# Performance work log

Measured on AMD Instinct MI355X. Metric: run time of the kernel, lower is better.

Reference implementation:

```python
import jax, jax.numpy as jnp
import numpy as np

N = 50000          # nodes
E = 400000         # edges (avg degree 8)
F_IN = 128
F_OUT = 128
H = 4
C = F_OUT // H     # 32
SCALE = np.sqrt(C).astype(np.float32)
EPS = 1e-5


def _linear_params(key, fan_out, fan_in):
    # torch nn.Linear default init: U(-1/sqrt(fan_in), 1/sqrt(fan_in))
    bound = 1.0 / np.sqrt(fan_in)
    kw, kb = jax.random.split(key)
    W = jax.random.uniform(kw, (fan_out, fan_in), minval=-bound, maxval=bound, dtype=jnp.float32)
    b = jax.random.uniform(kb, (fan_out,), minval=-bound, maxval=bound, dtype=jnp.float32)
    return W, b


def setup_inputs() -> dict:
    key = jax.random.key(0)
    ks = jax.random.split(key, 12)
    Wq, bq = _linear_params(ks[0], F_OUT, F_IN)
    Wk, bk = _linear_params(ks[1], F_OUT, F_IN)
    Wv, bv = _linear_params(ks[2], F_OUT, F_IN)
    We, be = _linear_params(ks[3], F_OUT, F_IN)
    Wev, bev = _linear_params(ks[4], F_OUT, F_IN)
    Wout, bout = _linear_params(ks[5], F_OUT, F_OUT)
    node_feats = jax.random.normal(ks[6], (N, F_IN), dtype=jnp.float32)
    edge_feats = jax.random.normal(ks[7], (E, F_IN), dtype=jnp.float32)
    src = jax.random.randint(ks[8], (E,), 0, N, dtype=jnp.int32)
    dst = jax.random.randint(ks[9], (E,), 0, N, dtype=jnp.int32)
    return {
        'node_feats': node_feats, 'edge_feats': edge_feats,
        'src': src, 'dst': dst,
        'Wq': Wq, 'bq': bq, 'Wk': Wk, 'bk': bk, 'Wv': Wv, 'bv': bv,
        'We': We, 'be': be, 'Wev': Wev, 'bev': bev, 'Wout': Wout, 'bout': bout,
        'ln_ng': jnp.ones((F_OUT,), jnp.float32), 'ln_nb': jnp.zeros((F_OUT,), jnp.float32),
        'ln_eg': jnp.ones((F_OUT,), jnp.float32), 'ln_eb': jnp.zeros((F_OUT,), jnp.float32),
    }


def _layernorm(x, g, b):
    mu = jnp.mean(x, axis=-1, keepdims=True)
    var = jnp.var(x, axis=-1, keepdims=True)
    return (x - mu) * jax.lax.rsqrt(var + EPS) * g + b


def reference(node_feats, edge_feats, src, dst,
              Wq, bq, Wk, bk, Wv, bv, We, be, Wev, bev, Wout, bout,
              ln_ng, ln_nb, ln_eg, ln_eb):
    # per-node projections, viewed as [N, H, C]
    q = (node_feats @ Wq.T + bq).reshape(N, H, C)
    k = (node_feats @ Wk.T + bk).reshape(N, H, C)
    v = (node_feats @ Wv.T + bv).reshape(N, H, C)
    e = (edge_feats @ We.T + be).reshape(E, H, C)

    # u_dot_v('q','k','score'): per-edge per-head dot -> [E, H, 1]
    score = jnp.einsum('ehc,ehc->eh', q[src], k[dst])[:, :, None]
    m = score / SCALE + e                       # broadcast -> [E, H, C]
    # NOTE: faithful to original — softmax over the HEADS axis (dim=1)
    attn = jax.nn.softmax(m, axis=1)            # [E, H, C]

    # u_mul_e + sum aggregation at destination
    msg = v[src] * attn                         # [E, H, C]
    agg = jax.ops.segment_sum(msg, dst, num_segments=N)   # [N, H, C]

    x = agg.reshape(N, H * C)
    y = m.reshape(E, H * C)
    x = jax.nn.silu(_layernorm(x, ln_ng, ln_nb))
    y = jax.nn.silu(_layernorm(y, ln_eg, ln_eb))
    # residual
    x = (node_feats @ Wout.T + bout) + x
    y = (edge_feats @ Wev.T + bev) + y
    return (x, y)
```

## Files before the change

### kernel.cpp

```cpp
#include <hip/hip_runtime.h>
#include <math.h>

#define NN 50000
#define NE 400000
#define FDIM 128

constexpr float INV_SCALE = 0.17677669529663687f;
constexpr float LN_EPS = 1e-5f;

typedef short bf16x8 __attribute__((ext_vector_type(8)));
typedef float f32x4 __attribute__((ext_vector_type(4)));

static __device__ __forceinline__ short f2bf(float f) {
    unsigned u = __builtin_bit_cast(unsigned, f);
    u += 0x7FFFu + ((u >> 16) & 1u);
    return (short)(u >> 16);
}
static __device__ __forceinline__ float bf2f(short h) {
    unsigned u = ((unsigned)(unsigned short)h) << 16;
    return __builtin_bit_cast(float, u);
}

static __device__ __forceinline__ void load_afrags(const short* At, int w, int l, bf16x8* a) {
    int lr = l & 15, lq = l >> 4;
    int arow = w * 16 + lr;
#pragma unroll
    for (int ks = 0; ks < 4; ++ks) {
        int ch = ks * 4 + lq;
        a[ks] = *(const bf16x8*)(At + arow * FDIM + ((ch ^ (arow & 7)) * 8));
    }
}

static __device__ __forceinline__ void mfma_gemm(const bf16x8* a,
                                                 const short* __restrict__ W,
                                                 const float* __restrict__ bias,
                                                 int lr, int lq, f32x4* acc) {
#pragma unroll
    for (int n = 0; n < 8; ++n) {
        float bb = bias[n * 16 + lr];
        f32x4 t; t[0] = bb; t[1] = bb; t[2] = bb; t[3] = bb;
        acc[n] = t;
#pragma unroll
        for (int ks = 0; ks < 4; ++ks) {
            bf16x8 b = *(const bf16x8*)(W + (n * 16 + lr) * FDIM + ks * 32 + lq * 8);
            acc[n] = __builtin_amdgcn_mfma_f32_16x16x32_bf16(a[ks], b, acc[n], 0, 0, 0);
        }
    }
}

__global__ __launch_bounds__(256) void convert_weights(
    const float* __restrict__ w0, const float* __restrict__ w1,
    const float* __restrict__ w2, const float* __restrict__ w3,
    const float* __restrict__ w4, const float* __restrict__ w5,
    short* __restrict__ out) {
    int idx = blockIdx.x * 256 + threadIdx.x;
    const float* srcs[6] = {w0, w1, w2, w3, w4, w5};
    out[idx] = f2bf(srcs[idx >> 14][idx & 16383]);
}

__global__ __launch_bounds__(256) void hist_kernel(const int* __restrict__ dst,
                                                   int* __restrict__ hist) {
    int e = blockIdx.x * 256 + threadIdx.x;
    if (e < NE) atomicAdd(&hist[dst[e]], 1);
}

__global__ __launch_bounds__(256) void scan_kernel(const int* __restrict__ hist,
                                                   int* __restrict__ cursor) {
    __shared__ int wsum[4];
    __shared__ int srun;
    int tid = threadIdx.x;
    int lane = tid & 63, w = tid >> 6;
    if (tid == 0) srun = 0;
    __syncthreads();
    for (int base = 0; base < NN; base += 256) {
        int i = base + tid;
        int v = (i < NN) ? hist[i] : 0;
        int inc = v;
#pragma unroll
        for (int off = 1; off < 64; off <<= 1) {
            int t = __shfl_up(inc, off);
            if (lane >= off) inc += t;
        }
        if (lane == 63) wsum[w] = inc;
        __syncthreads();
        int wo = 0;
        for (int j = 0; j < w; ++j) wo += wsum[j];
        int run = srun;
        if (i < NN) cursor[i] = run + wo + inc - v;
        __syncthreads();
        if (tid == 255) srun = run + wo + inc;
        __syncthreads();
    }
}

__global__ __launch_bounds__(256) void scatter_kernel(const int* __restrict__ dst,
                                                      int* __restrict__ cursor,
                                                      int* __restrict__ sidx) {
    int e = blockIdx.x * 256 + threadIdx.x;
    if (e < NE) sidx[atomicAdd(&cursor[dst[e]], 1)] = e;
}

__global__ __launch_bounds__(256) void node_proj_kernel(
    const float* __restrict__ nf,
    const short* __restrict__ wq16, const short* __restrict__ wk16,
    const short* __restrict__ wv16, const short* __restrict__ wo16,
    const float* __restrict__ bq, const float* __restrict__ bk,
    const float* __restrict__ bv, const float* __restrict__ bo,
    short* __restrict__ q, short* __restrict__ k, short* __restrict__ v,
    float* __restrict__ xout) {
    __shared__ __align__(16) short At[64 * FDIM];
    int m0  = blockIdx.x * 64;
    int tid = threadIdx.x;
#pragma unroll
    for (int j = 0; j < 4; ++j) {
        int row = (tid >> 4) + j * 16;
        int g   = tid & 15;
        int m   = m0 + row;
        float4 a0 = make_float4(0.f, 0.f, 0.f, 0.f);
        float4 a1 = make_float4(0.f, 0.f, 0.f, 0.f);
        if (m < NN) {
            const float4* p = (const float4*)(nf + (size_t)m * FDIM + g * 8);
            a0 = p[0]; a1 = p[1];
        }
        bf16x8 h;
        h[0] = f2bf(a0.x); h[1] = f2bf(a0.y); h[2] = f2bf(a0.z); h[3] = f2bf(a0.w);
        h[4] = f2bf(a1.x); h[5] = f2bf(a1.y); h[6] = f2bf(a1.z); h[7] = f2bf(a1.w);
        *(bf16x8*)(At + row * FDIM + ((g ^ (row & 7)) * 8)) = h;
    }
    __syncthreads();
    int w = tid >> 6, l = tid & 63;
    int lr = l & 15, lq = l >> 4;
    bf16x8 a[4];
    load_afrags(At, w, l, a);
    f32x4 acc[8];
    const short* Ws[3] = {wq16, wk16, wv16};
    const float* Bs[3] = {bq, bk, bv};
    short*       Os[3] = {q, k, v};
#pragma unroll
    for (int t = 0; t < 3; ++t) {
        mfma_gemm(a, Ws[t], Bs[t], lr, lq, acc);
#pragma unroll
        for (int n = 0; n < 8; ++n)
#pragma unroll
            for (int r = 0; r < 4; ++r) {
                int m = m0 + w * 16 + lq * 4 + r;
                if (m < NN) Os[t][(size_t)m * FDIM + n * 16 + lr] = f2bf(acc[n][r]);
            }
    }
    mfma_gemm(a, wo16, bo, lr, lq, acc);
#pragma unroll
    for (int n = 0; n < 8; ++n)
#pragma unroll
        for (int r = 0; r < 4; ++r) {
            int m = m0 + w * 16 + lq * 4 + r;
            if (m < NN) xout[(size_t)m * FDIM + n * 16 + lr] = acc[n][r];
        }
}

__global__ __launch_bounds__(256) void edge_kernel(
    const float* __restrict__ ef, const int* __restrict__ src, const int* __restrict__ dst,
    const int* __restrict__ sidx,
    const short* __restrict__ we16, const short* __restrict__ wev16,
    const float* __restrict__ be, const float* __restrict__ bev,
    const short* __restrict__ qbf, const short* __restrict__ kbf, const short* __restrict__ vbf,
    const float* __restrict__ ln_eg, const float* __restrict__ ln_eb,
    float* __restrict__ agg, float* __restrict__ yout) {
    __shared__ __align__(16) short At[64 * FDIM];
    __shared__ __align__(16) float sc[64 * 4];
    __shared__ int oL[64], sL[64], dL[64];
    int e0  = blockIdx.x * 64;
    int tid = threadIdx.x;

#pragma unroll
    for (int j = 0; j < 4; ++j) {
        int row = (tid >> 4) + j * 16;
        int g   = tid & 15;
        int o   = sidx[e0 + row];
        const float4* p = (const float4*)(ef + (size_t)o * FDIM + g * 8);
        float4 a0 = p[0], a1 = p[1];
        bf16x8 h;
        h[0] = f2bf(a0.x); h[1] = f2bf(a0.y); h[2] = f2bf(a0.z); h[3] = f2bf(a0.w);
        h[4] = f2bf(a1.x); h[5] = f2bf(a1.y); h[6] = f2bf(a1.z); h[7] = f2bf(a1.w);
        *(bf16x8*)(At + row * FDIM + ((g ^ (row & 7)) * 8)) = h;
    }

    int w = tid >> 6, l = tid & 63;
    {
        int eidx = w * 16 + (l >> 2);
        int h    = l & 3;
        int o    = sidx[e0 + eidx];
        int se = src[o], de = dst[o];
        if (h == 0) { oL[eidx] = o; sL[eidx] = se; dL[eidx] = de; }
        const bf16x8* qp = (const bf16x8*)(qbf + (size_t)se * FDIM + h * 32);
        const bf16x8* kp = (const bf16x8*)(kbf + (size_t)de * FDIM + h * 32);
        float s = 0.f;
#pragma unroll
        for (int i = 0; i < 4; ++i) {
            bf16x8 qa = qp[i], ka = kp[i];
#pragma unroll
            for (int jj = 0; jj < 8; ++jj) s += bf2f(qa[jj]) * bf2f(ka[jj]);
        }
        sc[eidx * 4 + h] = s * INV_SCALE;
    }
    __syncthreads();

    int lr = l & 15, lq = l >> 4;
    bf16x8 a[4];
    load_afrags(At, w, l, a);
    __syncthreads();

    f32x4 me[8], mvv[8];
    mfma_gemm(a, we16, be, lr, lq, me);
    mfma_gemm(a, wev16, bev, lr, lq, mvv);

    int rowb = w * 16 + lq * 4;
    float sr[4][4];
#pragma unroll
    for (int r = 0; r < 4; ++r) {
        f32x4 t = *(const f32x4*)(sc + (rowb + r) * 4);
        sr[r][0] = t[0]; sr[r][1] = t[1]; sr[r][2] = t[2]; sr[r][3] = t[3];
    }
#pragma unroll
    for (int n = 0; n < 8; ++n)
#pragma unroll
        for (int r = 0; r < 4; ++r)
            me[n][r] += sr[r][n >> 1];

    short* attnL = At;
#pragma unroll
    for (int r = 0; r < 4; ++r) {
#pragma unroll
        for (int half = 0; half < 2; ++half) {
            float v0 = me[half][r],     v1 = me[half + 2][r];
            float v2 = me[half + 4][r], v3 = me[half + 6][r];
            float mx = fmaxf(fmaxf(v0, v1), fmaxf(v2, v3));
            float x0 = __expf(v0 - mx), x1 = __expf(v1 - mx);
            float x2 = __expf(v2 - mx), x3 = __expf(v3 - mx);
            float inv = 1.f / (x0 + x1 + x2 + x3);
            float at[4] = {x0 * inv, x1 * inv, x2 * inv, x3 * inv};
#pragma unroll
            for (int h = 0; h < 4; ++h)
                attnL[(rowb + r) * FDIM + (2 * h + half) * 16 + lr] = f2bf(at[h]);
        }
    }

#pragma unroll
    for (int r = 0; r < 4; ++r) {
        float sum1 = 0.f, sum2 = 0.f;
#pragma unroll
        for (int n = 0; n < 8; ++n) { float t = me[n][r]; sum1 += t; sum2 += t * t; }
#pragma unroll
        for (int off = 1; off < 16; off <<= 1) {
            sum1 += __shfl_xor(sum1, off);
            sum2 += __shfl_xor(sum2, off);
        }
        float mean = sum1 * (1.f / 128.f);
        float var  = sum2 * (1.f / 128.f) - mean * mean;
        float rstd = rsqrtf(var + LN_EPS);
        int orow = oL[rowb + r];
#pragma unroll
        for (int n = 0; n < 8; ++n) {
            int col = n * 16 + lr;
            float t  = (me[n][r] - mean) * rstd * ln_eg[col] + ln_eb[col];
            float si = t / (1.f + __expf(-t));
            yout[(size_t)orow * FDIM + col] = si + mvv[n][r];
        }
    }
    __syncthreads();

    {
        int c  = tid & 127;
        int hh = tid >> 7;
        int j0 = hh * 32, j1 = j0 + 32;
        float acc = 0.f;
        int cur = dL[j0];
        for (int j = j0; j < j1; ++j) {
            int d = dL[j];
            if (d != cur) {
                unsafeAtomicAdd(&agg[(size_t)cur * FDIM + c], acc);
                acc = 0.f; cur = d;
            }
            float vv = bf2f(vbf[(size_t)sL[j] * FDIM + c]);
            float aa = bf2f(attnL[j * FDIM + c]);
            acc += vv * aa;
        }
        unsafeAtomicAdd(&agg[(size_t)cur * FDIM + c], acc);
    }
}

__global__ __launch_bounds__(256) void node_epilogue(
    const float* __restrict__ agg,
    const float* __restrict__ ln_ng, const float* __restrict__ ln_nb,
    float* __restrict__ xout) {
    int row = blockIdx.x * 4 + (threadIdx.x >> 6);
    if (row >= NN) return;
    int l = threadIdx.x & 63;
    float2 aa = *(const float2*)(agg + (size_t)row * FDIM + l * 2);
    float sum1 = aa.x + aa.y, sum2 = aa.x * aa.x + aa.y * aa.y;
#pragma unroll
    for (int off = 1; off < 64; off <<= 1) {
        sum1 += __shfl_xor(sum1, off);
        sum2 += __shfl_xor(sum2, off);
    }
    float mean = sum1 * (1.f / 128.f);
    float var  = sum2 * (1.f / 128.f) - mean * mean;
    float rstd = rsqrtf(var + LN_EPS);
    float2 gg = *(const float2*)(ln_ng + l * 2);
    float2 bb = *(const float2*)(ln_nb + l * 2);
    float t0 = (aa.x - mean) * rstd * gg.x + bb.x;
    float t1 = (aa.y - mean) * rstd * gg.y + bb.y;
    float s0 = t0 / (1.f + __expf(-t0));
    float s1 = t1 / (1.f + __expf(-t1));
    float2 o = *(const float2*)(xout + (size_t)row * FDIM + l * 2);
    o.x += s0;
    o.y += s1;
    *(float2*)(xout + (size_t)row * FDIM + l * 2) = o;
}

extern "C" void kernel_launch(void* const* d_in, const int* in_sizes, int n_in,
                              void* d_out, int out_size, void* d_ws, size_t ws_size,
                              hipStream_t stream) {
    const float* nf   = (const float*)d_in[0];
    const float* ef   = (const float*)d_in[1];
    const int*   src  = (const int*)d_in[2];
    const int*   dst  = (const int*)d_in[3];
    const float* Wq   = (const float*)d_in[4];  const float* bq   = (const float*)d_in[5];
    const float* Wk   = (const float*)d_in[6];  const float* bk   = (const float*)d_in[7];
    const float* Wv   = (const float*)d_in[8];  const float* bv   = (const float*)d_in[9];
    const float* We   = (const float*)d_in[10]; const float* be   = (const float*)d_in[11];
    const float* Wev  = (const float*)d_in[12]; const float* bev  = (const float*)d_in[13];
    const float* Wout = (const float*)d_in[14]; const float* bout = (const float*)d_in[15];
    const float* ln_ng = (const float*)d_in[16]; const float* ln_nb = (const float*)d_in[17];
    const float* ln_eg = (const float*)d_in[18]; const float* ln_eb = (const float*)d_in[19];

    float* xout = (float*)d_out;
    float* yout = xout + (size_t)NN * FDIM;

    char* ws = (char*)d_ws;
    short* qbf  = (short*)ws;                                   ws += (size_t)NN * FDIM * 2;
    short* kbf  = (short*)ws;                                   ws += (size_t)NN * FDIM * 2;
    short* vbf  = (short*)ws;                                   ws += (size_t)NN * FDIM * 2;
    float* agg  = (float*)ws;                                   ws += (size_t)NN * FDIM * 4;
    short* w16  = (short*)ws;                                   ws += (size_t)6 * 16384 * 2;
    int*   hist = (int*)ws;                                     ws += (size_t)NN * 4;
    int*   curs = (int*)ws;                                     ws += (size_t)NN * 4;
    int*   sidx = (int*)ws;                                     ws += (size_t)NE * 4;
    short* wq16  = w16;
    short* wk16  = w16 + 16384;
    short* wv16  = w16 + 32768;
    short* we16  = w16 + 49152;
    short* wev16 = w16 + 65536;
    short* wo16  = w16 + 81920;

    hipMemsetAsync(agg, 0, (size_t)NN * FDIM * sizeof(float), stream);
    hipMemsetAsync(hist, 0, (size_t)NN * sizeof(int), stream);
    convert_weights<<<384, 256, 0, stream>>>(Wq, Wk, Wv, We, Wev, Wout, w16);
    hist_kernel<<<(NE + 255) / 256, 256, 0, stream>>>(dst, hist);
    scan_kernel<<<1, 256, 0, stream>>>(hist, curs);
    scatter_kernel<<<(NE + 255) / 256, 256, 0, stream>>>(dst, curs, sidx);
    node_proj_kernel<<<(NN + 63) / 64, 256, 0, stream>>>(
        nf, wq16, wk16, wv16, wo16, bq, bk, bv, bout, qbf, kbf, vbf, xout);
    edge_kernel<<<NE / 64, 256, 0, stream>>>(
        ef, src, dst, sidx, we16, wev16, be, bev, qbf, kbf, vbf, ln_eg, ln_eb, agg, yout);
    node_epilogue<<<(NN + 3) / 4, 256, 0, stream>>>(agg, ln_ng, ln_nb, xout);
}
```

Measured before the change: 969.3 us.

## Replace atomic scatter aggregation with CSR pull-based node aggregation and parallel scan

The edge kernel now processes edges in original order, with coalesced edge-feature reads and output writes, and stores bf16 attention weights to a workspace buffer. A new node kernel pulls messages per destination node through the CSR index and fuses the sum with the layernorm epilogue. This removes the float atomics, the agg memset and the permuted edge writes. The single-block serial scan is replaced by a three-kernel parallel scan. In exchange it writes and re-reads roughly 100MB of attention data and adds dependent gather loads per edge in the node kernel.

```diff
diff --git a/kernel.cpp b/kernel.cpp
--- a/kernel.cpp
+++ b/kernel.cpp
@@ -4,6 +4,7 @@
 #define NN 50000
 #define NE 400000
 #define FDIM 128
+#define NB 196
 
 constexpr float INV_SCALE = 0.17677669529663687f;
 constexpr float LN_EPS = 1e-5f;
@@ -64,32 +65,52 @@
     if (e < NE) atomicAdd(&hist[dst[e]], 1);
 }
 
-__global__ __launch_bounds__(256) void scan_kernel(const int* __restrict__ hist,
-                                                   int* __restrict__ cursor) {
+__global__ __launch_bounds__(256) void scanA_kernel(const int* __restrict__ hist,
+                                                    int* __restrict__ row_start,
+                                                    int* __restrict__ bsum) {
     __shared__ int wsum[4];
-    __shared__ int srun;
-    int tid = threadIdx.x;
-    int lane = tid & 63, w = tid >> 6;
-    if (tid == 0) srun = 0;
-    __syncthreads();
-    for (int base = 0; base < NN; base += 256) {
-        int i = base + tid;
-        int v = (i < NN) ? hist[i] : 0;
-        int inc = v;
-#pragma unroll
-        for (int off = 1; off < 64; off <<= 1) {
-            int t = __shfl_up(inc, off);
-            if (lane >= off) inc += t;
-        }
-        if (lane == 63) wsum[w] = inc;
-        __syncthreads();
-        int wo = 0;
-        for (int j = 0; j < w; ++j) wo += wsum[j];
-        int run = srun;
-        if (i < NN) cursor[i] = run + wo + inc - v;
-        __syncthreads();
-        if (tid == 255) srun = run + wo + inc;
-        __syncthreads();
+    int tid = threadIdx.x, lane = tid & 63, w = tid >> 6;
+    int i = blockIdx.x * 256 + tid;
+    int v = (i < NN) ? hist[i] : 0;
+    int inc = v;
+#pragma unroll
+    for (int off = 1; off < 64; off <<= 1) {
+        int t = __shfl_up(inc, off);
+        if (lane >= off) inc += t;
+    }
+    if (lane == 63) wsum[w] = inc;
+    __syncthreads();
+    int wo = 0;
+    for (int j = 0; j < w; ++j) wo += wsum[j];
+    if (i < NN) row_start[i] = wo + inc - v;
+    if (tid == 255) bsum[blockIdx.x] = wo + inc;
+}
+
+__global__ __launch_bounds__(256) void scanB_kernel(int* __restrict__ bsum) {
+    __shared__ int wsum[4];
+    int tid = threadIdx.x, lane = tid & 63, w = tid >> 6;
+    int v = (tid < NB) ? bsum[tid] : 0;
+    int inc = v;
+#pragma unroll
+    for (int off = 1; off < 64; off <<= 1) {
+        int t = __shfl_up(inc, off);
+        if (lane >= off) inc += t;
+    }
+    if (lane == 63) wsum[w] = inc;
+    __syncthreads();
+    int wo = 0;
+    for (int j = 0; j < w; ++j) wo += wsum[j];
+    if (tid < NB) bsum[tid] = wo + inc - v;
+}
+
+__global__ __launch_bounds__(256) void scanC_kernel(int* __restrict__ row_start,
+                                                    const int* __restrict__ bsum,
+                                                    int* __restrict__ cursor) {
+    int i = blockIdx.x * 256 + threadIdx.x;
+    if (i < NN) {
+        int s = row_start[i] + bsum[blockIdx.x];
+        row_start[i] = s;
+        cursor[i] = s;
     }
 }
 
@@ -157,17 +178,15 @@
         }
 }
 
-__global__ __launch_bounds__(256) void edge_kernel(
+__global__ __launch_bounds__(256) void edge_m_kernel(
     const float* __restrict__ ef, const int* __restrict__ src, const int* __restrict__ dst,
-    const int* __restrict__ sidx,
     const short* __restrict__ we16, const short* __restrict__ wev16,
     const float* __restrict__ be, const float* __restrict__ bev,
-    const short* __restrict__ qbf, const short* __restrict__ kbf, const short* __restrict__ vbf,
+    const short* __restrict__ qbf, const short* __restrict__ kbf,
     const float* __restrict__ ln_eg, const float* __restrict__ ln_eb,
-    float* __restrict__ agg, float* __restrict__ yout) {
+    short* __restrict__ attn, float* __restrict__ yout) {
     __shared__ __align__(16) short At[64 * FDIM];
     __shared__ __align__(16) float sc[64 * 4];
-    __shared__ int oL[64], sL[64], dL[64];
     int e0  = blockIdx.x * 64;
     int tid = threadIdx.x;
 
@@ -175,8 +194,7 @@
     for (int j = 0; j < 4; ++j) {
         int row = (tid >> 4) + j * 16;
         int g   = tid & 15;
-        int o   = sidx[e0 + row];
-        const float4* p = (const float4*)(ef + (size_t)o * FDIM + g * 8);
+        const float4* p = (const float4*)(ef + (size_t)(e0 + row) * FDIM + g * 8);
         float4 a0 = p[0], a1 = p[1];
         bf16x8 h;
         h[0] = f2bf(a0.x); h[1] = f2bf(a0.y); h[2] = f2bf(a0.z); h[3] = f2bf(a0.w);
@@ -188,9 +206,8 @@
     {
         int eidx = w * 16 + (l >> 2);
         int h    = l & 3;
-        int o    = sidx[e0 + eidx];
-        int se = src[o], de = dst[o];
-        if (h == 0) { oL[eidx] = o; sL[eidx] = se; dL[eidx] = de; }
+        int eg   = e0 + eidx;
+        int se = src[eg], de = dst[eg];
         const bf16x8* qp = (const bf16x8*)(qbf + (size_t)se * FDIM + h * 32);
         const bf16x8* kp = (const bf16x8*)(kbf + (size_t)de * FDIM + h * 32);
         float s = 0.f;
@@ -214,17 +231,13 @@
     mfma_gemm(a, wev16, bev, lr, lq, mvv);
 
     int rowb = w * 16 + lq * 4;
-    float sr[4][4];
 #pragma unroll
     for (int r = 0; r < 4; ++r) {
         f32x4 t = *(const f32x4*)(sc + (rowb + r) * 4);
-        sr[r][0] = t[0]; sr[r][1] = t[1]; sr[r][2] = t[2]; sr[r][3] = t[3];
-    }
-#pragma unroll
-    for (int n = 0; n < 8; ++n)
-#pragma unroll
-        for (int r = 0; r < 4; ++r)
-            me[n][r] += sr[r][n >> 1];
+#pragma unroll
+        for (int n = 0; n < 8; ++n)
+            me[n][r] += ((const float*)&t)[n >> 1];
+    }
 
     short* attnL = At;
 #pragma unroll
@@ -257,46 +270,52 @@
         float mean = sum1 * (1.f / 128.f);
         float var  = sum2 * (1.f / 128.f) - mean * mean;
         float rstd = rsqrtf(var + LN_EPS);
-        int orow = oL[rowb + r];
+        int eg = e0 + rowb + r;
 #pragma unroll
         for (int n = 0; n < 8; ++n) {
             int col = n * 16 + lr;
             float t  = (me[n][r] - mean) * rstd * ln_eg[col] + ln_eb[col];
             float si = t / (1.f + __expf(-t));
-            yout[(size_t)orow * FDIM + col] = si + mvv[n][r];
-        }
-    }
-    __syncthreads();
-
-    {
-        int c  = tid & 127;
-        int hh = tid >> 7;
-        int j0 = hh * 32, j1 = j0 + 32;
-        float acc = 0.f;
-        int cur = dL[j0];
-        for (int j = j0; j < j1; ++j) {
-            int d = dL[j];
-            if (d != cur) {
-                unsafeAtomicAdd(&agg[(size_t)cur * FDIM + c], acc);
-                acc = 0.f; cur = d;
-            }
-            float vv = bf2f(vbf[(size_t)sL[j] * FDIM + c]);
-            float aa = bf2f(attnL[j * FDIM + c]);
-            acc += vv * aa;
-        }
-        unsafeAtomicAdd(&agg[(size_t)cur * FDIM + c], acc);
-    }
-}
-
-__global__ __launch_bounds__(256) void node_epilogue(
-    const float* __restrict__ agg,
+            yout[(size_t)eg * FDIM + col] = si + mvv[n][r];
+        }
+    }
+    __syncthreads();
+
+#pragma unroll
+    for (int j = 0; j < 4; ++j) {
+        int row = (tid >> 4) + j * 16;
+        int g   = tid & 15;
+        *(bf16x8*)(attn + (size_t)(e0 + row) * FDIM + g * 8) =
+            *(const bf16x8*)(attnL + row * FDIM + g * 8);
+    }
+}
+
+__global__ __launch_bounds__(256) void node_agg_kernel(
+    const int* __restrict__ row_start, const int* __restrict__ hist,
+    const int* __restrict__ sidx, const int* __restrict__ src,
+    const short* __restrict__ attn, const short* __restrict__ vbf,
     const float* __restrict__ ln_ng, const float* __restrict__ ln_nb,
     float* __restrict__ xout) {
-    int row = blockIdx.x * 4 + (threadIdx.x >> 6);
-    if (row >= NN) return;
-    int l = threadIdx.x & 63;
-    float2 aa = *(const float2*)(agg + (size_t)row * FDIM + l * 2);
-    float sum1 = aa.x + aa.y, sum2 = aa.x * aa.x + aa.y * aa.y;
+    int tid = threadIdx.x;
+    int w = tid >> 6, l = tid & 63;
+    int n = blockIdx.x * 4 + w;
+    if (n >= NN) return;
+    int start = row_start[n];
+    int deg   = hist[n];
+    float a0 = 0.f, a1 = 0.f;
+    for (int j = 0; j < deg; ++j) {
+        int e = sidx[start + j];
+        int s = src[e];
+        unsigned av = *(const unsigned*)(attn + (size_t)e * FDIM + l * 2);
+        unsigned vv = *(const unsigned*)(vbf  + (size_t)s * FDIM + l * 2);
+        float alo = __builtin_bit_cast(float, av << 16);
+        float ahi = __builtin_bit_cast(float, av & 0xFFFF0000u);
+        float vlo = __builtin_bit_cast(float, vv << 16);
+        float vhi = __builtin_bit_cast(float, vv & 0xFFFF0000u);
+        a0 += alo * vlo;
+        a1 += ahi * vhi;
+    }
+    float sum1 = a0 + a1, sum2 = a0 * a0 + a1 * a1;
 #pragma unroll
     for (int off = 1; off < 64; off <<= 1) {
         sum1 += __shfl_xor(sum1, off);
@@ -307,14 +326,14 @@
     float rstd = rsqrtf(var + LN_EPS);
     float2 gg = *(const float2*)(ln_ng + l * 2);
     float2 bb = *(const float2*)(ln_nb + l * 2);
-    float t0 = (aa.x - mean) * rstd * gg.x + bb.x;
-    float t1 = (aa.y - mean) * rstd * gg.y + bb.y;
+    float t0 = (a0 - mean) * rstd * gg.x + bb.x;
+    float t1 = (a1 - mean) * rstd * gg.y + bb.y;
     float s0 = t0 / (1.f + __expf(-t0));
     float s1 = t1 / (1.f + __expf(-t1));
-    float2 o = *(const float2*)(xout + (size_t)row * FDIM + l * 2);
+    float2 o = *(const float2*)(xout + (size_t)n * FDIM + l * 2);
     o.x += s0;
     o.y += s1;
-    *(float2*)(xout + (size_t)row * FDIM + l * 2) = o;
+    *(float2*)(xout + (size_t)n * FDIM + l * 2) = o;
 }
 
 extern "C" void kernel_launch(void* const* d_in, const int* in_sizes, int n_in,
@@ -337,14 +356,16 @@
     float* yout = xout + (size_t)NN * FDIM;
 
     char* ws = (char*)d_ws;
-    short* qbf  = (short*)ws;                                   ws += (size_t)NN * FDIM * 2;
-    short* kbf  = (short*)ws;                                   ws += (size_t)NN * FDIM * 2;
-    short* vbf  = (short*)ws;                                   ws += (size_t)NN * FDIM * 2;
-    float* agg  = (float*)ws;                                   ws += (size_t)NN * FDIM * 4;
-    short* w16  = (short*)ws;                                   ws += (size_t)6 * 16384 * 2;
-    int*   hist = (int*)ws;                                     ws += (size_t)NN * 4;
-    int*   curs = (int*)ws;                                     ws += (size_t)NN * 4;
-    int*   sidx = (int*)ws;                                     ws += (size_t)NE * 4;
+    short* qbf  = (short*)ws;   ws += (size_t)NN * FDIM * 2;
+    short* kbf  = (short*)ws;   ws += (size_t)NN * FDIM * 2;
+    short* vbf  = (short*)ws;   ws += (size_t)NN * FDIM * 2;
+    short* attn = (short*)ws;   ws += (size_t)NE * FDIM * 2;
+    short* w16  = (short*)ws;   ws += (size_t)6 * 16384 * 2;
+    int*   hist = (int*)ws;     ws += (size_t)NN * 4;
+    int*   rows = (int*)ws;     ws += (size_t)NN * 4;
+    int*   curs = (int*)ws;     ws += (size_t)NN * 4;
+    int*   sidx = (int*)ws;     ws += (size_t)NE * 4;
+    int*   bsum = (int*)ws;     ws += (size_t)NB * 4;
     short* wq16  = w16;
     short* wk16  = w16 + 16384;
     short* wv16  = w16 + 32768;
@@ -352,15 +373,17 @@
     short* wev16 = w16 + 65536;
     short* wo16  = w16 + 81920;
 
-    hipMemsetAsync(agg, 0, (size_t)NN * FDIM * sizeof(float), stream);
     hipMemsetAsync(hist, 0, (size_t)NN * sizeof(int), stream);
     convert_weights<<<384, 256, 0, stream>>>(Wq, Wk, Wv, We, Wev, Wout, w16);
     hist_kernel<<<(NE + 255) / 256, 256, 0, stream>>>(dst, hist);
-    scan_kernel<<<1, 256, 0, stream>>>(hist, curs);
+    scanA_kernel<<<NB, 256, 0, stream>>>(hist, rows, bsum);
+    scanB_kernel<<<1, 256, 0, stream>>>(bsum);
+    scanC_kernel<<<NB, 256, 0, stream>>>(rows, bsum, curs);
     scatter_kernel<<<(NE + 255) / 256, 256, 0, stream>>>(dst, curs, sidx);
     node_proj_kernel<<<(NN + 63) / 64, 256, 0, stream>>>(
         nf, wq16, wk16, wv16, wo16, bq, bk, bv, bout, qbf, kbf, vbf, xout);
-    edge_kernel<<<NE / 64, 256, 0, stream>>>(
-        ef, src, dst, sidx, we16, wev16, be, bev, qbf, kbf, vbf, ln_eg, ln_eb, agg, yout);
-    node_epilogue<<<(NN + 3) / 4, 256, 0, stream>>>(agg, ln_ng, ln_nb, xout);
-}
+    edge_m_kernel<<<NE / 64, 256, 0, stream>>>(
+        ef, src, dst, we16, wev16, be, bev, qbf, kbf, ln_eg, ln_eb, attn, yout);
+    node_agg_kernel<<<(NN + 3) / 4, 256, 0, stream>>>(
+        rows, hist, sidx, src, attn, vbf, ln_ng, ln_nb, xout);
+}
```

Result: faster. 856.2 us (-11.7%).
